# Performance work log

Measured on AMD Instinct MI355X. Metric: run time of the kernel, lower is better.

Reference implementation:

```python
import jax, jax.numpy as jnp
import numpy as np

SEQ_LEN = 8192
INPUT_SIZE = 2048
HIDDEN_SIZE = 2048


def _xavier(key, out_f, in_f):
    # xavier_uniform_ bound = sqrt(6 / (fan_in + fan_out))
    bound = np.sqrt(6.0 / (in_f + out_f)).astype(np.float32)
    return jax.random.uniform(key, (out_f, in_f), jnp.float32, -bound, bound)


def setup_inputs() -> dict:
    key = jax.random.key(0)
    k_x, k_wi, k_bi, k_wh, k_bh = jax.random.split(key, 5)
    x = jax.random.normal(k_x, (SEQ_LEN, INPUT_SIZE), jnp.float32)
    Wi = _xavier(k_wi, HIDDEN_SIZE, INPUT_SIZE)
    bi = jax.random.uniform(k_bi, (HIDDEN_SIZE,), jnp.float32)
    Wh = _xavier(k_wh, HIDDEN_SIZE, HIDDEN_SIZE)
    bh = jax.random.uniform(k_bh, (HIDDEN_SIZE,), jnp.float32)
    return {"x": x, "Wi": Wi, "bi": bi, "Wh": Wh, "bh": bh}


def reference(x, Wi, bi, Wh, bh):
    # Precompute the input projection for all timesteps as one GEMM: [S, H]
    x_proj = x @ Wi.T + bi

    def step(h, xt):
        # h_t = tanh(i2h(x_t) + h2h(h_{t-1}))
        h_new = jnp.tanh(xt + h @ Wh.T + bh)
        return h_new, h_new

    h0 = jnp.zeros((Wh.shape[0],), dtype=x.dtype)
    h_n, outputs = jax.lax.scan(step, h0, x_proj)
    # outputs: [S, H] hidden states; h_n: [H] final hidden state
    return outputs, h_n
```

## Files before the change

### kernel.cpp

```cpp
#include <hip/hip_runtime.h>
#include <hip/hip_bf16.h>

#define SEQ 8192
#define HID 2048
#define NBLK 64
#define ROWS 32

typedef short short8 __attribute__((ext_vector_type(8)));
typedef float floatx4 __attribute__((ext_vector_type(4)));
typedef unsigned uintx4 __attribute__((ext_vector_type(4)));

__device__ __forceinline__ void split_bf16(const float* __restrict__ p,
                                           short8& hi, short8& lo) {
    const float4 f0 = *(const float4*)p;
    const float4 f1 = *(const float4*)(p + 4);
    const float f[8] = {f0.x, f0.y, f0.z, f0.w, f1.x, f1.y, f1.z, f1.w};
#pragma unroll
    for (int e = 0; e < 8; ++e) {
        const unsigned u = __float_as_uint(f[e]);
        const unsigned r = (u + 0x7fffu + ((u >> 16) & 1u)) & 0xffff0000u;
        hi[e] = (short)(r >> 16);
        const float l = f[e] - __uint_as_float(r);
        const unsigned ul = __float_as_uint(l);
        lo[e] = (short)((ul + 0x7fffu + ((ul >> 16) & 1u)) >> 16);
    }
}

__global__ __launch_bounds__(256) void xproj_gemm(
    const float* __restrict__ x,
    const float* __restrict__ Wi,
    const float* __restrict__ bi,
    float* __restrict__ xp)
{
    const int bn = blockIdx.x;
    const int bm = blockIdx.y;
    const int tid = threadIdx.x;
    const int wave = tid >> 6;
    const int lane = tid & 63;
    const int wM = wave & 1, wN = wave >> 1;
    const int l16 = lane & 15, kq = lane >> 4;
    const int m0 = bm * 64 + wM * 32;
    const int n0 = bn * 64 + wN * 32;

    floatx4 acc00 = {0.f,0.f,0.f,0.f}, acc01 = {0.f,0.f,0.f,0.f};
    floatx4 acc10 = {0.f,0.f,0.f,0.f}, acc11 = {0.f,0.f,0.f,0.f};

    const float* xA0 = x  + (size_t)(m0 + l16)      * HID;
    const float* xA1 = x  + (size_t)(m0 + 16 + l16) * HID;
    const float* wB0 = Wi + (size_t)(n0 + l16)      * HID;
    const float* wB1 = Wi + (size_t)(n0 + 16 + l16) * HID;

    for (int kc = 0; kc < HID; kc += 32) {
        const int k = kc + kq * 8;
        short8 a0h, a0l, a1h, a1l, b0h, b0l, b1h, b1l;
        split_bf16(xA0 + k, a0h, a0l);
        split_bf16(xA1 + k, a1h, a1l);
        split_bf16(wB0 + k, b0h, b0l);
        split_bf16(wB1 + k, b1h, b1l);
        acc00 = __builtin_amdgcn_mfma_f32_16x16x32_bf16(a0h, b0h, acc00, 0,0,0);
        acc00 = __builtin_amdgcn_mfma_f32_16x16x32_bf16(a0l, b0h, acc00, 0,0,0);
        acc00 = __builtin_amdgcn_mfma_f32_16x16x32_bf16(a0h, b0l, acc00, 0,0,0);
        acc01 = __builtin_amdgcn_mfma_f32_16x16x32_bf16(a0h, b1h, acc01, 0,0,0);
        acc01 = __builtin_amdgcn_mfma_f32_16x16x32_bf16(a0l, b1h, acc01, 0,0,0);
        acc01 = __builtin_amdgcn_mfma_f32_16x16x32_bf16(a0h, b1l, acc01, 0,0,0);
        acc10 = __builtin_amdgcn_mfma_f32_16x16x32_bf16(a1h, b0h, acc10, 0,0,0);
        acc10 = __builtin_amdgcn_mfma_f32_16x16x32_bf16(a1l, b0h, acc10, 0,0,0);
        acc10 = __builtin_amdgcn_mfma_f32_16x16x32_bf16(a1h, b0l, acc10, 0,0,0);
        acc11 = __builtin_amdgcn_mfma_f32_16x16x32_bf16(a1h, b1h, acc11, 0,0,0);
        acc11 = __builtin_amdgcn_mfma_f32_16x16x32_bf16(a1l, b1h, acc11, 0,0,0);
        acc11 = __builtin_amdgcn_mfma_f32_16x16x32_bf16(a1h, b1l, acc11, 0,0,0);
    }

    const float bi0 = bi[n0 + l16];
    const float bi1 = bi[n0 + 16 + l16];
#pragma unroll
    for (int reg = 0; reg < 4; ++reg) {
        const int mlo = m0 + kq * 4 + reg;
        const int mhi = mlo + 16;
        xp[(size_t)mlo * HID + n0 + l16]      = acc00[reg] + bi0;
        xp[(size_t)mlo * HID + n0 + 16 + l16] = acc01[reg] + bi1;
        xp[(size_t)mhi * HID + n0 + l16]      = acc10[reg] + bi0;
        xp[(size_t)mhi * HID + n0 + 16 + l16] = acc11[reg] + bi1;
    }
}

__global__ __launch_bounds__(512, 1) void rnn_scan(
    const float* __restrict__ Wh,
    const float* __restrict__ bh,
    const float* __restrict__ xp,
    unsigned long long* hbuf,
    float* out)
{
    __shared__ float h_lds[HID];

    const int b   = blockIdx.x;
    const int tid = threadIdx.x;
    const int wv  = tid >> 6;
    const int L   = tid & 63;
    const int row = b * ROWS + wv * 4 + L;

    floatx4 w[4][8];
#pragma unroll
    for (int r = 0; r < 4; ++r) {
        const size_t rr = (size_t)(b * ROWS + wv * 4 + r);
#pragma unroll
        for (int j = 0; j < 8; ++j)
            w[r][j] = *(const floatx4*)(Wh + rr * HID + 256 * j + 4 * L);
    }
    const float bh_l = (L < 4) ? bh[row] : 0.f;

    float xp_cur = (L < 4) ? xp[row] : 0.f;
    float prev_h = 0.f;

    for (int t = 0; t < SEQ; ++t) {
        float acc[4] = {0.f, 0.f, 0.f, 0.f};

        if (t > 0) {
            const unsigned long long* src = hbuf + ((t - 1) & 1) * HID;
            const unsigned want = (unsigned)(t - 1);
            const unsigned long long* s0 = src + 2 * tid;
            const unsigned long long* s1 = src + 1024 + 2 * tid;
            uintx4 p0, p1;
            do {
                asm volatile(
                    "global_load_dwordx4 %0, %2, off sc0 sc1\n\t"
                    "global_load_dwordx4 %1, %3, off sc0 sc1\n\t"
                    "s_waitcnt vmcnt(0)"
                    : "=&v"(p0), "=&v"(p1)
                    : "v"(s0), "v"(s1)
                    : "memory");
            } while ((p0[1] != want) | (p0[3] != want) |
                     (p1[1] != want) | (p1[3] != want));
            *(float2*)&h_lds[2 * tid] =
                make_float2(__uint_as_float(p0[0]), __uint_as_float(p0[2]));
            *(float2*)&h_lds[1024 + 2 * tid] =
                make_float2(__uint_as_float(p1[0]), __uint_as_float(p1[2]));
            if (L < 4) out[(size_t)(t - 1) * HID + row] = prev_h;
            asm volatile("s_waitcnt lgkmcnt(0)\n\ts_barrier" ::: "memory");
        }

        float xp_next = 0.f;
        if (L < 4 && t + 1 < SEQ) xp_next = xp[(size_t)(t + 1) * HID + row];

        if (t > 0) {
#pragma unroll
            for (int j = 0; j < 8; ++j) {
                const float4 hv = *(const float4*)&h_lds[256 * j + 4 * L];
#pragma unroll
                for (int r = 0; r < 4; ++r) {
                    acc[r] += w[r][j][0] * hv.x;
                    acc[r] += w[r][j][1] * hv.y;
                    acc[r] += w[r][j][2] * hv.z;
                    acc[r] += w[r][j][3] * hv.w;
                }
            }
        }

#pragma unroll
        for (int off = 32; off > 0; off >>= 1) {
#pragma unroll
            for (int r = 0; r < 4; ++r) acc[r] += __shfl_xor(acc[r], off, 64);
        }

        if (L < 4) {
            float a = acc[L] + xp_cur + bh_l;
            a = fminf(fmaxf(a, -15.f), 15.f);
            const float e = __expf(2.f * a);
            const float hval = (e - 1.f) / (e + 1.f);
            const unsigned long long tagged =
                ((unsigned long long)(unsigned)t << 32) |
                (unsigned long long)__float_as_uint(hval);
            __hip_atomic_store(&hbuf[(t & 1) * HID + row], tagged,
                               __ATOMIC_RELAXED, __HIP_MEMORY_SCOPE_AGENT);
            prev_h = hval;
        }
        xp_cur = xp_next;
    }

    if (L < 4) {
        out[(size_t)(SEQ - 1) * HID + row] = prev_h;
        out[(size_t)SEQ * HID + row]       = prev_h;
    }
}

extern "C" void kernel_launch(void* const* d_in, const int* in_sizes, int n_in,
                              void* d_out, int out_size, void* d_ws, size_t ws_size,
                              hipStream_t stream) {
    const float* x  = (const float*)d_in[0];
    const float* Wi = (const float*)d_in[1];
    const float* bi = (const float*)d_in[2];
    const float* Wh = (const float*)d_in[3];
    const float* bh = (const float*)d_in[4];
    float* out      = (float*)d_out;

    float* xp = (float*)d_ws;
    unsigned long long* hbuf = (unsigned long long*)(xp + (size_t)SEQ * HID);

    xproj_gemm<<<dim3(HID / 64, SEQ / 64), 256, 0, stream>>>(x, Wi, bi, xp);
    rnn_scan<<<NBLK, 512, 0, stream>>>(Wh, bh, xp, hbuf, out);
}
```

Baseline: 20.64 ms.

## Pack two hidden values per tagged 64-bit word to halve polling traffic

Measured after the change: 21.52 ms. +4.3%, slower.

```diff
diff --git a/kernel.cpp b/kernel.cpp
--- a/kernel.cpp
+++ b/kernel.cpp
@@ -84,6 +84,18 @@
     }
 }
 
+
+__device__ __forceinline__ unsigned long long pack2(float h0, float h1,
+                                                    unsigned tag) {
+    const unsigned u0 = __float_as_uint(h0);
+    const unsigned u1 = __float_as_uint(h1);
+    const unsigned r0 = (u0 + 0x3Fu + ((u0 >> 7) & 1u)) >> 7;
+    const unsigned r1 = (u1 + 0x3Fu + ((u1 >> 7) & 1u)) >> 7;
+    return ((unsigned long long)tag << 51) |
+           ((unsigned long long)r0 << 25) |
+           (unsigned long long)r1;
+}
+
 __global__ __launch_bounds__(512, 1) void rnn_scan(
     const float* __restrict__ Wh,
     const float* __restrict__ bh,
@@ -116,25 +128,24 @@
         float acc[4] = {0.f, 0.f, 0.f, 0.f};
 
         if (t > 0) {
-            const unsigned long long* src = hbuf + ((t - 1) & 1) * HID;
+            const unsigned long long* src =
+                hbuf + ((t - 1) & 1) * 1024 + 2 * tid;
             const unsigned want = (unsigned)(t - 1);
-            const unsigned long long* s0 = src + 2 * tid;
-            const unsigned long long* s1 = src + 1024 + 2 * tid;
-            uintx4 p0, p1;
+            uintx4 p;
             do {
                 asm volatile(
-                    "global_load_dwordx4 %0, %2, off sc0 sc1\n\t"
-                    "global_load_dwordx4 %1, %3, off sc0 sc1\n\t"
+                    "global_load_dwordx4 %0, %1, off sc0 sc1\n\t"
                     "s_waitcnt vmcnt(0)"
-                    : "=&v"(p0), "=&v"(p1)
-                    : "v"(s0), "v"(s1)
+                    : "=&v"(p)
+                    : "v"(src)
                     : "memory");
-            } while ((p0[1] != want) | (p0[3] != want) |
-                     (p1[1] != want) | (p1[3] != want));
-            *(float2*)&h_lds[2 * tid] =
-                make_float2(__uint_as_float(p0[0]), __uint_as_float(p0[2]));
-            *(float2*)&h_lds[1024 + 2 * tid] =
-                make_float2(__uint_as_float(p1[0]), __uint_as_float(p1[2]));
+            } while (((p[1] >> 19) != want) | ((p[3] >> 19) != want));
+            float4 hv;
+            hv.x = __uint_as_float((p[1] << 14) | ((p[0] >> 25) << 7));
+            hv.y = __uint_as_float(p[0] << 7);
+            hv.z = __uint_as_float((p[3] << 14) | ((p[2] >> 25) << 7));
+            hv.w = __uint_as_float(p[2] << 7);
+            *(float4*)&h_lds[4 * tid] = hv;
             if (L < 4) out[(size_t)(t - 1) * HID + row] = prev_h;
             asm volatile("s_waitcnt lgkmcnt(0)\n\ts_barrier" ::: "memory");
         }
@@ -167,11 +178,14 @@
             a = fminf(fmaxf(a, -15.f), 15.f);
             const float e = __expf(2.f * a);
             const float hval = (e - 1.f) / (e + 1.f);
-            const unsigned long long tagged =
-                ((unsigned long long)(unsigned)t << 32) |
-                (unsigned long long)__float_as_uint(hval);
-            __hip_atomic_store(&hbuf[(t & 1) * HID + row], tagged,
-                               __ATOMIC_RELAXED, __HIP_MEMORY_SCOPE_AGENT);
+            const float hpartner = __shfl_xor(hval, 1, 64);
+            if ((L & 1) == 0) {
+                const unsigned long long w64 =
+                    pack2(hval, hpartner, (unsigned)t);
+                __hip_atomic_store(
+                    &hbuf[(t & 1) * 1024 + b * 16 + wv * 2 + (L >> 1)], w64,
+                    __ATOMIC_RELAXED, __HIP_MEMORY_SCOPE_AGENT);
+            }
             prev_h = hval;
         }
         xp_cur = xp_next;
```

## Pipeline hidden-state polling with async global-to-LDS loads in a ring

Applied to the files above, without the earlier changes.

New measurement: 37.54 ms. 1.82x slower.

```diff
diff --git a/kernel.cpp b/kernel.cpp
--- a/kernel.cpp
+++ b/kernel.cpp
@@ -5,10 +5,14 @@
 #define HID 2048
 #define NBLK 64
 #define ROWS 32
+#define DEPTH 4
 
 typedef short short8 __attribute__((ext_vector_type(8)));
 typedef float floatx4 __attribute__((ext_vector_type(4)));
 typedef unsigned uintx4 __attribute__((ext_vector_type(4)));
+
+typedef const __attribute__((address_space(1))) void* gas_ptr;
+typedef __attribute__((address_space(3))) void* las_ptr;
 
 __device__ __forceinline__ void split_bf16(const float* __restrict__ p,
                                            short8& hi, short8& lo) {
@@ -92,6 +96,7 @@
     float* out)
 {
     __shared__ float h_lds[HID];
+    __shared__ __align__(16) unsigned long long scr[8][DEPTH][256];
 
     const int b   = blockIdx.x;
     const int tid = threadIdx.x;
@@ -112,29 +117,64 @@
     float xp_cur = (L < 4) ? xp[row] : 0.f;
     float prev_h = 0.f;
 
+    auto issue = [&](const char* gbase, int slot) {
+        __builtin_amdgcn_global_load_lds(
+            (gas_ptr)(const void*)(gbase + 16 * L),
+            (las_ptr)(void*)&scr[wv][slot][0], 16, 0, 17);
+        __builtin_amdgcn_global_load_lds(
+            (gas_ptr)(const void*)(gbase + 8192 + 16 * L),
+            (las_ptr)(void*)&scr[wv][slot][128], 16, 0, 17);
+    };
+
     for (int t = 0; t < SEQ; ++t) {
         float acc[4] = {0.f, 0.f, 0.f, 0.f};
 
         if (t > 0) {
-            const unsigned long long* src = hbuf + ((t - 1) & 1) * HID;
             const unsigned want = (unsigned)(t - 1);
-            const unsigned long long* s0 = src + 2 * tid;
-            const unsigned long long* s1 = src + 1024 + 2 * tid;
-            uintx4 p0, p1;
-            do {
-                asm volatile(
-                    "global_load_dwordx4 %0, %2, off sc0 sc1\n\t"
-                    "global_load_dwordx4 %1, %3, off sc0 sc1\n\t"
-                    "s_waitcnt vmcnt(0)"
-                    : "=&v"(p0), "=&v"(p1)
-                    : "v"(s0), "v"(s1)
-                    : "memory");
-            } while ((p0[1] != want) | (p0[3] != want) |
-                     (p1[1] != want) | (p1[3] != want));
-            *(float2*)&h_lds[2 * tid] =
-                make_float2(__uint_as_float(p0[0]), __uint_as_float(p0[2]));
-            *(float2*)&h_lds[1024 + 2 * tid] =
-                make_float2(__uint_as_float(p1[0]), __uint_as_float(p1[2]));
+            const char* g = (const char*)(hbuf + ((t - 1) & 1) * HID) + 1024 * wv;
+            issue(g, 1); issue(g, 2); issue(g, 3);
+            int slot = 0, spins = 0;
+            for (;;) {
+                asm volatile("s_waitcnt vmcnt(6)" ::: "memory");
+                const unsigned long long v0 = scr[wv][slot][L];
+                const unsigned long long v1 = scr[wv][slot][64 + L];
+                const unsigned long long v2 = scr[wv][slot][128 + L];
+                const unsigned long long v3 = scr[wv][slot][192 + L];
+                const bool ok = ((unsigned)(v0 >> 32) == want) &
+                                ((unsigned)(v1 >> 32) == want) &
+                                ((unsigned)(v2 >> 32) == want) &
+                                ((unsigned)(v3 >> 32) == want);
+                if (__all(ok)) {
+                    h_lds[128 * wv + L]             = __uint_as_float((unsigned)v0);
+                    h_lds[128 * wv + 64 + L]        = __uint_as_float((unsigned)v1);
+                    h_lds[1024 + 128 * wv + L]      = __uint_as_float((unsigned)v2);
+                    h_lds[1024 + 128 * wv + 64 + L] = __uint_as_float((unsigned)v3);
+                    break;
+                }
+                if (++spins > 64) {
+                    const unsigned long long* src = hbuf + ((t - 1) & 1) * HID;
+                    const unsigned long long* s0 = src + 2 * tid;
+                    const unsigned long long* s1 = src + 1024 + 2 * tid;
+                    uintx4 p0, p1;
+                    do {
+                        asm volatile(
+                            "global_load_dwordx4 %0, %2, off sc0 sc1\n\t"
+                            "global_load_dwordx4 %1, %3, off sc0 sc1\n\t"
+                            "s_waitcnt vmcnt(0)"
+                            : "=&v"(p0), "=&v"(p1)
+                            : "v"(s0), "v"(s1)
+                            : "memory");
+                    } while ((p0[1] != want) | (p0[3] != want) |
+                             (p1[1] != want) | (p1[3] != want));
+                    *(float2*)&h_lds[2 * tid] = make_float2(
+                        __uint_as_float(p0[0]), __uint_as_float(p0[2]));
+                    *(float2*)&h_lds[1024 + 2 * tid] = make_float2(
+                        __uint_as_float(p1[0]), __uint_as_float(p1[2]));
+                    break;
+                }
+                issue(g, slot);
+                slot = (slot + 1) & (DEPTH - 1);
+            }
             if (L < 4) out[(size_t)(t - 1) * HID + row] = prev_h;
             asm volatile("s_waitcnt lgkmcnt(0)\n\ts_barrier" ::: "memory");
         }
@@ -166,13 +206,19 @@
             float a = acc[L] + xp_cur + bh_l;
             a = fminf(fmaxf(a, -15.f), 15.f);
             const float e = __expf(2.f * a);
-            const float hval = (e - 1.f) / (e + 1.f);
+            prev_h = (e - 1.f) / (e + 1.f);
+        }
+
+        if (t + 1 < SEQ) {
+            const char* gn = (const char*)(hbuf + (t & 1) * HID) + 1024 * wv;
+            issue(gn, 0);
+        }
+        if (L < 4) {
             const unsigned long long tagged =
                 ((unsigned long long)(unsigned)t << 32) |
-                (unsigned long long)__float_as_uint(hval);
+                (unsigned long long)__float_as_uint(prev_h);
             __hip_atomic_store(&hbuf[(t & 1) * HID + row], tagged,
                                __ATOMIC_RELAXED, __HIP_MEMORY_SCOPE_AGENT);
-            prev_h = hval;
         }
         xp_cur = xp_next;
     }
```

## Replace per-step block barrier with per-wave LDS flags and ring buffers

Applied to the files above, without the earlier changes.

Result: slower. 26.22 ms (+27.1%).

```diff
diff --git a/kernel.cpp b/kernel.cpp
--- a/kernel.cpp
+++ b/kernel.cpp
@@ -91,7 +91,8 @@
     unsigned long long* hbuf,
     float* out)
 {
-    __shared__ float h_lds[HID];
+    __shared__ float h_lds[2][HID];
+    __shared__ unsigned flags[2][8];
 
     const int b   = blockIdx.x;
     const int tid = threadIdx.x;
@@ -99,6 +100,9 @@
     const int L   = tid & 63;
     const int row = b * ROWS + wv * 4 + L;
 
+    if (tid < 16) flags[tid >> 3][tid & 7] = 0xFFFFFFFFu;
+    __syncthreads();
+
     floatx4 w[4][8];
 #pragma unroll
     for (int r = 0; r < 4; ++r) {
@@ -114,10 +118,11 @@
 
     for (int t = 0; t < SEQ; ++t) {
         float acc[4] = {0.f, 0.f, 0.f, 0.f};
+        const int q = (t - 1) & 1;
+        const unsigned want = (unsigned)(t - 1);
 
         if (t > 0) {
-            const unsigned long long* src = hbuf + ((t - 1) & 1) * HID;
-            const unsigned want = (unsigned)(t - 1);
+            const unsigned long long* src = hbuf + (size_t)((t - 1) & 3) * HID;
             const unsigned long long* s0 = src + 2 * tid;
             const unsigned long long* s1 = src + 1024 + 2 * tid;
             uintx4 p0, p1;
@@ -131,27 +136,70 @@
                     : "memory");
             } while ((p0[1] != want) | (p0[3] != want) |
                      (p1[1] != want) | (p1[3] != want));
-            *(float2*)&h_lds[2 * tid] =
+            *(float2*)&h_lds[q][2 * tid] =
                 make_float2(__uint_as_float(p0[0]), __uint_as_float(p0[2]));
-            *(float2*)&h_lds[1024 + 2 * tid] =
+            *(float2*)&h_lds[q][1024 + 2 * tid] =
                 make_float2(__uint_as_float(p1[0]), __uint_as_float(p1[2]));
+            asm volatile("s_waitcnt lgkmcnt(0)" ::: "memory");
+            if (L == 0) flags[q][wv] = want;
             if (L < 4) out[(size_t)(t - 1) * HID + row] = prev_h;
-            asm volatile("s_waitcnt lgkmcnt(0)\n\ts_barrier" ::: "memory");
         }
 
         float xp_next = 0.f;
         if (L < 4 && t + 1 < SEQ) xp_next = xp[(size_t)(t + 1) * HID + row];
 
         if (t > 0) {
-#pragma unroll
-            for (int j = 0; j < 8; ++j) {
-                const float4 hv = *(const float4*)&h_lds[256 * j + 4 * L];
+            const unsigned long long* src = hbuf + (size_t)((t - 1) & 3) * HID;
+#pragma unroll
+            for (int p = 0; p < 4; ++p) {
+                volatile unsigned* vf = &flags[q][2 * p];
+                int spins = 0;
+                bool flagged = true;
+                while ((vf[0] != want) | (vf[1] != want)) {
+                    if (++spins > 16384) { flagged = false; break; }
+                }
+                asm volatile("" ::: "memory");
+                float4 hv0, hv1;
+                if (flagged) {
+                    hv0 = *(const float4*)&h_lds[q][256 * p + 4 * L];
+                    hv1 = *(const float4*)&h_lds[q][1024 + 256 * p + 4 * L];
+                } else {
+                    const unsigned long long* c0 = src + 256 * p + 4 * L;
+                    const unsigned long long* c1 = src + 1024 + 256 * p + 4 * L;
+                    uintx4 a0, a1, b0, b1;
+                    do {
+                        asm volatile(
+                            "global_load_dwordx4 %0, %4, off sc0 sc1\n\t"
+                            "global_load_dwordx4 %1, %4, off offset:16 sc0 sc1\n\t"
+                            "global_load_dwordx4 %2, %5, off sc0 sc1\n\t"
+                            "global_load_dwordx4 %3, %5, off offset:16 sc0 sc1\n\t"
+                            "s_waitcnt vmcnt(0)"
+                            : "=&v"(a0), "=&v"(a1), "=&v"(b0), "=&v"(b1)
+                            : "v"(c0), "v"(c1)
+                            : "memory");
+                    } while ((a0[1] != want) | (a0[3] != want) |
+                             (a1[1] != want) | (a1[3] != want) |
+                             (b0[1] != want) | (b0[3] != want) |
+                             (b1[1] != want) | (b1[3] != want));
+                    hv0 = make_float4(__uint_as_float(a0[0]),
+                                      __uint_as_float(a0[2]),
+                                      __uint_as_float(a1[0]),
+                                      __uint_as_float(a1[2]));
+                    hv1 = make_float4(__uint_as_float(b0[0]),
+                                      __uint_as_float(b0[2]),
+                                      __uint_as_float(b1[0]),
+                                      __uint_as_float(b1[2]));
+                }
 #pragma unroll
                 for (int r = 0; r < 4; ++r) {
-                    acc[r] += w[r][j][0] * hv.x;
-                    acc[r] += w[r][j][1] * hv.y;
-                    acc[r] += w[r][j][2] * hv.z;
-                    acc[r] += w[r][j][3] * hv.w;
+                    acc[r] += w[r][p][0] * hv0.x;
+                    acc[r] += w[r][p][1] * hv0.y;
+                    acc[r] += w[r][p][2] * hv0.z;
+                    acc[r] += w[r][p][3] * hv0.w;
+                    acc[r] += w[r][p + 4][0] * hv1.x;
+                    acc[r] += w[r][p + 4][1] * hv1.y;
+                    acc[r] += w[r][p + 4][2] * hv1.z;
+                    acc[r] += w[r][p + 4][3] * hv1.w;
                 }
             }
         }
@@ -170,7 +218,7 @@
             const unsigned long long tagged =
                 ((unsigned long long)(unsigned)t << 32) |
                 (unsigned long long)__float_as_uint(hval);
-            __hip_atomic_store(&hbuf[(t & 1) * HID + row], tagged,
+            __hip_atomic_store(&hbuf[(size_t)(t & 3) * HID + row], tagged,
                                __ATOMIC_RELAXED, __HIP_MEMORY_SCOPE_AGENT);
             prev_h = hval;
         }
```
